# Kernel tuning notes

Measured on AMD Instinct MI355X. Metric: run time of the kernel, lower is better.

Reference implementation:

```python
import jax, jax.numpy as jnp
import numpy as np

WINDOW_LEN = 512
N_VAR = 64
LOW_RANK = 16
BATCH = 512


def setup_inputs() -> dict:
    key = jax.random.key(0)
    k_x, k_g, k_b, k_A, k_B = jax.random.split(key, 5)
    x = jax.random.normal(k_x, (BATCH, WINDOW_LEN, N_VAR, 1), dtype=jnp.float32)
    # gating initialized at gating_init in the module; use small positive values
    gating = 0.01 * jnp.ones((N_VAR,), dtype=jnp.float32)
    # bias initialized to zeros in the module, but give it random values so the
    # residual path is exercised numerically
    bias = 0.02 * jax.random.normal(k_b, (WINDOW_LEN, N_VAR), dtype=jnp.float32)
    # kaiming-uniform-ish scale for lora_A: bound = sqrt(6 / fan_in) / sqrt(1+a^2) with a=sqrt(5)
    bound = np.sqrt(6.0 / LOW_RANK) / np.sqrt(6.0)
    lora_A = jax.random.uniform(k_A, (WINDOW_LEN, LOW_RANK), dtype=jnp.float32,
                                minval=-bound, maxval=bound)
    # lora_B is zero-init in the module; use small random values for a nontrivial test
    lora_B = 0.02 * jax.random.normal(k_B, (LOW_RANK, WINDOW_LEN, N_VAR), dtype=jnp.float32)
    return {"x": x, "gating": gating, "bias": bias, "lora_A": lora_A, "lora_B": lora_B}


def reference(x, gating, bias, lora_A, lora_B):
    # x: [b, t, n, d] with t == window_len and n*d == n_var (var_wise=True path)
    b, t, n, d = x.shape
    xr = x.reshape(b, t, n * d)                     # [b, t, v]
    x1 = jnp.tanh(gating * xr)                      # gate per variable, [b, t, v]
    # Original computes weight = einsum('ik,kjl->ijl', lora_A, lora_B)  (dense [t,t,v])
    # then einsum('biv,iov->bov', x1, weight). Same math via associativity:
    tmp = jnp.einsum('biv,ik->bkv', x1, lora_A)     # [b, r, v]
    new_x = jnp.einsum('bkv,kov->bov', tmp, lora_B) # [b, t, v]
    out = xr + new_x + bias                          # residual + bias
    return out.reshape(b, t, n, d)
```

## Files before the change

kernel.cpp:

```cpp
#include <hip/hip_runtime.h>

#define WL 512
#define NV 64
#define LR 16
#define NB 512

__device__ __forceinline__ float tanh_fast(float x) {
    float e = __expf(2.0f * x);
    return 1.0f - 2.0f / (e + 1.0f);
}

__global__ __launch_bounds__(1024, 8) void k_tmp(
    const float* __restrict__ x, const float* __restrict__ gating,
    const float* __restrict__ A, float* __restrict__ tmp)
{
    __shared__ float red[16 * LR * NV];
    const int tid = threadIdx.x;
    const int b = blockIdx.x;

    const int v = tid & 63;
    const int tg = __builtin_amdgcn_readfirstlane(tid >> 6);
    const float g = gating[v];

    float acc[LR];
#pragma unroll
    for (int k = 0; k < LR; ++k) acc[k] = 0.f;

    const float* xb = x + (size_t)b * (WL * NV) + (size_t)tg * 32 * NV + v;
    const float* Abase = A + (size_t)tg * 32 * LR;

#pragma unroll 4
    for (int i = 0; i < 32; ++i) {
        const float x1 = tanh_fast(g * xb[i * NV]);
        const float* Ar = Abase + i * LR;
#pragma unroll
        for (int k = 0; k < LR; ++k) acc[k] = fmaf(x1, Ar[k], acc[k]);
    }

#pragma unroll
    for (int k = 0; k < LR; ++k) red[(tg * LR + k) * NV + v] = acc[k];
    __syncthreads();

    {
        const int p = tid;
        float s = 0.f;
#pragma unroll
        for (int t = 0; t < 16; ++t) s += red[t * (LR * NV) + p];
        tmp[(size_t)b * (LR * NV) + p] = s;
    }
}

__global__ __launch_bounds__(512, 8) void k_out(
    const float* __restrict__ x, const float* __restrict__ bias,
    const float* __restrict__ Bm, const float* __restrict__ tmp,
    float* __restrict__ out)
{
    const int tid = threadIdx.x;
    const int v = tid & 63;
    const int og = tid >> 6;
    const int o_base = blockIdx.y * 16 + og * 2;
    const int b0 = blockIdx.x * 8;

    float Breg[2][LR];
#pragma unroll
    for (int j = 0; j < 2; ++j) {
        const int o = o_base + j;
#pragma unroll
        for (int k = 0; k < LR; ++k)
            Breg[j][k] = Bm[((size_t)k * WL + o) * NV + v];
    }
    float breg[2];
#pragma unroll
    for (int j = 0; j < 2; ++j) breg[j] = bias[(o_base + j) * NV + v];

    for (int bi = 0; bi < 8; ++bi) {
        const int b = b0 + bi;
        const float* tb = tmp + (size_t)b * (LR * NV) + v;
        float tr[LR];
#pragma unroll
        for (int k = 0; k < LR; ++k) tr[k] = tb[k * NV];
        const float* xb = x + (size_t)b * WL * NV;
        float* ob = out + (size_t)b * WL * NV;
#pragma unroll
        for (int j = 0; j < 2; ++j) {
            const int o = o_base + j;
            float acc = breg[j];
#pragma unroll
            for (int k = 0; k < LR; ++k) acc += tr[k] * Breg[j][k];
            ob[o * NV + v] = xb[o * NV + v] + acc;
        }
    }
}

extern "C" void kernel_launch(void* const* d_in, const int* in_sizes, int n_in,
                              void* d_out, int out_size, void* d_ws, size_t ws_size,
                              hipStream_t stream) {
    const float* x      = (const float*)d_in[0];
    const float* gating = (const float*)d_in[1];
    const float* bias   = (const float*)d_in[2];
    const float* A      = (const float*)d_in[3];
    const float* Bm     = (const float*)d_in[4];
    float* out = (float*)d_out;
    float* tmp = (float*)d_ws;

    k_tmp<<<NB, 1024, 0, stream>>>(x, gating, A, tmp);
    k_out<<<dim3(64, 32), 512, 0, stream>>>(x, bias, Bm, tmp, out);
}
```

Measured before the change: 51.23 us.

## Retile k_out with 8 outputs per thread and double-buffered batch loads

Restructures the output kernel so each thread keeps 8 output rows of B in registers (up from 2) and handles 16 batches per block, with 4 waves per block instead of 8. Loads of tmp and x for the next batch are issued before computing the current one, a software double-buffer meant to hide global memory latency. Larger per-thread register tiles raise reuse of B and cut redundant B loads. In exchange register pressure rises and occupancy falls to 2 waves per EU, leaving fewer blocks to hide latency.

Measured after the change: 46.99 us. -8.3%, faster.

```diff
diff --git a/kernel.cpp b/kernel.cpp
--- a/kernel.cpp
+++ b/kernel.cpp
@@ -50,44 +50,84 @@
     }
 }
 
-__global__ __launch_bounds__(512, 8) void k_out(
+__global__ __attribute__((amdgpu_flat_work_group_size(256, 256),
+                          amdgpu_waves_per_eu(2, 2)))
+void k_out(
     const float* __restrict__ x, const float* __restrict__ bias,
     const float* __restrict__ Bm, const float* __restrict__ tmp,
     float* __restrict__ out)
 {
     const int tid = threadIdx.x;
     const int v = tid & 63;
-    const int og = tid >> 6;
-    const int o_base = blockIdx.y * 16 + og * 2;
-    const int b0 = blockIdx.x * 8;
+    const int w = tid >> 6;
+    const int o_base = blockIdx.y * 32 + w * 8;
+    const int b0 = blockIdx.x * 16;
 
-    float Breg[2][LR];
+    float Breg[8][LR];
 #pragma unroll
-    for (int j = 0; j < 2; ++j) {
+    for (int j = 0; j < 8; ++j) {
         const int o = o_base + j;
 #pragma unroll
         for (int k = 0; k < LR; ++k)
             Breg[j][k] = Bm[((size_t)k * WL + o) * NV + v];
     }
-    float breg[2];
+    float breg[8];
 #pragma unroll
-    for (int j = 0; j < 2; ++j) breg[j] = bias[(o_base + j) * NV + v];
+    for (int j = 0; j < 8; ++j) breg[j] = bias[(o_base + j) * NV + v];
 
-    for (int bi = 0; bi < 8; ++bi) {
+    float trA[LR], trB[LR], xrA[8], xrB[8];
+
+    {
+        const float* tb = tmp + (size_t)b0 * (LR * NV) + v;
+#pragma unroll
+        for (int k = 0; k < LR; ++k) trA[k] = tb[k * NV];
+        const float* xb = x + (size_t)b0 * WL * NV;
+#pragma unroll
+        for (int j = 0; j < 8; ++j) xrA[j] = xb[(o_base + j) * NV + v];
+    }
+
+#pragma unroll 1
+    for (int bi = 0; bi < 16; bi += 2) {
         const int b = b0 + bi;
-        const float* tb = tmp + (size_t)b * (LR * NV) + v;
-        float tr[LR];
+
+        {
+            const float* tb = tmp + (size_t)(b + 1) * (LR * NV) + v;
 #pragma unroll
-        for (int k = 0; k < LR; ++k) tr[k] = tb[k * NV];
-        const float* xb = x + (size_t)b * WL * NV;
-        float* ob = out + (size_t)b * WL * NV;
+            for (int k = 0; k < LR; ++k) trB[k] = tb[k * NV];
+            const float* xb = x + (size_t)(b + 1) * WL * NV;
 #pragma unroll
-        for (int j = 0; j < 2; ++j) {
-            const int o = o_base + j;
-            float acc = breg[j];
+            for (int j = 0; j < 8; ++j) xrB[j] = xb[(o_base + j) * NV + v];
+        }
+
+        {
+            float* ob = out + (size_t)b * WL * NV;
 #pragma unroll
-            for (int k = 0; k < LR; ++k) acc += tr[k] * Breg[j][k];
-            ob[o * NV + v] = xb[o * NV + v] + acc;
+            for (int j = 0; j < 8; ++j) {
+                float acc = breg[j];
+#pragma unroll
+                for (int k = 0; k < LR; ++k) acc += trA[k] * Breg[j][k];
+                ob[(o_base + j) * NV + v] = xrA[j] + acc;
+            }
+        }
+
+        if (bi + 2 < 16) {
+            const float* tb = tmp + (size_t)(b + 2) * (LR * NV) + v;
+#pragma unroll
+            for (int k = 0; k < LR; ++k) trA[k] = tb[k * NV];
+            const float* xb = x + (size_t)(b + 2) * WL * NV;
+#pragma unroll
+            for (int j = 0; j < 8; ++j) xrA[j] = xb[(o_base + j) * NV + v];
+        }
+
+        {
+            float* ob = out + (size_t)(b + 1) * WL * NV;
+#pragma unroll
+            for (int j = 0; j < 8; ++j) {
+                float acc = breg[j];
+#pragma unroll
+                for (int k = 0; k < LR; ++k) acc += trB[k] * Breg[j][k];
+                ob[(o_base + j) * NV + v] = xrB[j] + acc;
+            }
         }
     }
 }
@@ -104,5 +144,5 @@
     float* tmp = (float*)d_ws;
 
     k_tmp<<<NB, 1024, 0, stream>>>(x, gating, A, tmp);
-    k_out<<<dim3(64, 32), 512, 0, stream>>>(x, bias, Bm, tmp, out);
+    k_out<<<dim3(32, 16), 256, 0, stream>>>(x, bias, Bm, tmp, out);
 }
```

## Stage B and tmp tiles in LDS, prefetch x, shrink k_out blocks

Applied to the files above, without the earlier changes.

k_out now loads its B tile and the tmp rows for its batch group into shared memory using float4 global loads, then reads them per thread from LDS. The x value for the next batch is loaded one iteration early so the global load latency overlaps the current output computation. Blocks shrink to 256 threads covering 8 output rows, with twice as many blocks and a waves-per-EU hint. This adds LDS use, a block barrier and more blocks in exchange for wider, coalesced loads and fewer repeated global reads of tmp.

Measured after the change: 51.56 us. Within noise of the previous version (+0.6%).

```diff
diff --git a/kernel.cpp b/kernel.cpp
--- a/kernel.cpp
+++ b/kernel.cpp
@@ -4,6 +4,8 @@
 #define NV 64
 #define LR 16
 #define NB 512
+#define BB 8
+#define OO 8
 
 __device__ __forceinline__ float tanh_fast(float x) {
     float e = __expf(2.0f * x);
@@ -50,45 +52,79 @@
     }
 }
 
-__global__ __launch_bounds__(512, 8) void k_out(
+__global__ __attribute__((amdgpu_flat_work_group_size(256, 256),
+                          amdgpu_waves_per_eu(2, 2)))
+void k_out(
     const float* __restrict__ x, const float* __restrict__ bias,
     const float* __restrict__ Bm, const float* __restrict__ tmp,
     float* __restrict__ out)
 {
+    __shared__ float B_lds[OO * LR * NV];
+    __shared__ float T_lds[BB * LR * NV];
     const int tid = threadIdx.x;
     const int v = tid & 63;
-    const int og = tid >> 6;
-    const int o_base = blockIdx.y * 16 + og * 2;
-    const int b0 = blockIdx.x * 8;
+    const int wv = tid >> 6;
+    const int o0 = blockIdx.y * OO;
+    const int b0 = blockIdx.x * BB;
 
+#pragma unroll
+    for (int i = 0; i < 8; ++i) {
+        const int fidx = i * 256 + tid;
+        const int ko = fidx >> 4;
+        const int v4 = fidx & 15;
+        const int ol = ko >> 4;
+        const int k  = ko & 15;
+        const float4 val = *(const float4*)(Bm + ((size_t)k * WL + (o0 + ol)) * NV + v4 * 4);
+        *(float4*)(B_lds + ((ol * LR + k) * NV) + v4 * 4) = val;
+    }
+    {
+        const float4* src = (const float4*)(tmp + (size_t)b0 * (LR * NV));
+        float4* dst = (float4*)T_lds;
+#pragma unroll
+        for (int i = 0; i < 8; ++i) dst[i * 256 + tid] = src[i * 256 + tid];
+    }
+    __syncthreads();
+
+    const int ol0 = wv * 2;
     float Breg[2][LR];
 #pragma unroll
-    for (int j = 0; j < 2; ++j) {
-        const int o = o_base + j;
+    for (int j = 0; j < 2; ++j)
 #pragma unroll
         for (int k = 0; k < LR; ++k)
-            Breg[j][k] = Bm[((size_t)k * WL + o) * NV + v];
-    }
+            Breg[j][k] = B_lds[((ol0 + j) * LR + k) * NV + v];
     float breg[2];
 #pragma unroll
-    for (int j = 0; j < 2; ++j) breg[j] = bias[(o_base + j) * NV + v];
+    for (int j = 0; j < 2; ++j) breg[j] = bias[(o0 + ol0 + j) * NV + v];
 
-    for (int bi = 0; bi < 8; ++bi) {
-        const int b = b0 + bi;
-        const float* tb = tmp + (size_t)b * (LR * NV) + v;
+    float xr[2], xrn[2];
+    {
+        const float* xb = x + (size_t)b0 * (WL * NV);
+#pragma unroll
+        for (int j = 0; j < 2; ++j) xr[j] = xb[(o0 + ol0 + j) * NV + v];
+    }
+
+    for (int bl = 0; bl < BB; ++bl) {
+        const int b = b0 + bl;
+        if (bl + 1 < BB) {
+            const float* xb = x + (size_t)(b + 1) * (WL * NV);
+#pragma unroll
+            for (int j = 0; j < 2; ++j) xrn[j] = xb[(o0 + ol0 + j) * NV + v];
+        }
+
         float tr[LR];
 #pragma unroll
-        for (int k = 0; k < LR; ++k) tr[k] = tb[k * NV];
-        const float* xb = x + (size_t)b * WL * NV;
-        float* ob = out + (size_t)b * WL * NV;
+        for (int k = 0; k < LR; ++k) tr[k] = T_lds[(bl * LR + k) * NV + v];
+
+        float* ob = out + (size_t)b * (WL * NV);
 #pragma unroll
         for (int j = 0; j < 2; ++j) {
-            const int o = o_base + j;
             float acc = breg[j];
 #pragma unroll
             for (int k = 0; k < LR; ++k) acc += tr[k] * Breg[j][k];
-            ob[o * NV + v] = xb[o * NV + v] + acc;
+            ob[(o0 + ol0 + j) * NV + v] = xr[j] + acc;
         }
+
+        if (bl + 1 < BB) { xr[0] = xrn[0]; xr[1] = xrn[1]; }
     }
 }
 
@@ -104,5 +140,5 @@
     float* tmp = (float*)d_ws;
 
     k_tmp<<<NB, 1024, 0, stream>>>(x, gating, A, tmp);
-    k_out<<<dim3(64, 32), 512, 0, stream>>>(x, bias, Bm, tmp, out);
+    k_out<<<dim3(64, 64), 256, 0, stream>>>(x, bias, Bm, tmp, out);
 }
```

## Vectorize k_out with float4 lanes and double-buffer tmp loads across batches

Applied to the files above, without the earlier changes.

Rewrites the output kernel so each lane handles four variables through float4 loads and stores. Each block now covers 16 batches with 256 threads, and the tmp rows for the next batch are prefetched into registers while the current one is computed. The aim is fewer, wider memory instructions and hidden tmp load latency. The cost is higher register pressure (16 float4 for B plus two tmp buffers), with waves per EU forced to 2, which limits occupancy for a kernel bound by memory bandwidth.

After: 63.55 us. +24.0%, slower.

```diff
diff --git a/kernel.cpp b/kernel.cpp
--- a/kernel.cpp
+++ b/kernel.cpp
@@ -4,6 +4,7 @@
 #define NV 64
 #define LR 16
 #define NB 512
+#define BI 16
 
 __device__ __forceinline__ float tanh_fast(float x) {
     float e = __expf(2.0f * x);
@@ -50,44 +51,62 @@
     }
 }
 
-__global__ __launch_bounds__(512, 8) void k_out(
+__global__ __attribute__((amdgpu_flat_work_group_size(256, 256),
+                          amdgpu_waves_per_eu(2, 2)))
+void k_out(
     const float* __restrict__ x, const float* __restrict__ bias,
     const float* __restrict__ Bm, const float* __restrict__ tmp,
     float* __restrict__ out)
 {
     const int tid = threadIdx.x;
-    const int v = tid & 63;
-    const int og = tid >> 6;
-    const int o_base = blockIdx.y * 16 + og * 2;
-    const int b0 = blockIdx.x * 8;
+    const int lane = tid & 63;
+    const int w = tid >> 6;
+    const int oL = lane >> 4;
+    const int vq = lane & 15;
+    const int o = blockIdx.y * 16 + w * 4 + oL;
+    const int b0 = blockIdx.x * BI;
 
-    float Breg[2][LR];
+    float4 Breg[LR];
 #pragma unroll
-    for (int j = 0; j < 2; ++j) {
-        const int o = o_base + j;
+    for (int k = 0; k < LR; ++k)
+        Breg[k] = *(const float4*)(Bm + ((size_t)k * WL + o) * NV + vq * 4);
+
+    const float4 bias4 = *(const float4*)(bias + (size_t)o * NV + vq * 4);
+
+    float4 tA[LR], tB[LR];
+    {
+        const float* tb = tmp + (size_t)b0 * (LR * NV);
 #pragma unroll
-        for (int k = 0; k < LR; ++k)
-            Breg[j][k] = Bm[((size_t)k * WL + o) * NV + v];
+        for (int k = 0; k < LR; ++k) tA[k] = *(const float4*)(tb + k * NV + vq * 4);
     }
-    float breg[2];
+
+#pragma unroll 1
+    for (int bl = 0; bl < BI; ++bl) {
+        const int b = b0 + bl;
+
+        if (bl + 1 < BI) {
+            const float* tb = tmp + (size_t)(b + 1) * (LR * NV);
 #pragma unroll
-    for (int j = 0; j < 2; ++j) breg[j] = bias[(o_base + j) * NV + v];
+            for (int k = 0; k < LR; ++k) tB[k] = *(const float4*)(tb + k * NV + vq * 4);
+        }
 
-    for (int bi = 0; bi < 8; ++bi) {
-        const int b = b0 + bi;
-        const float* tb = tmp + (size_t)b * (LR * NV) + v;
-        float tr[LR];
+        const float4 x4 = *(const float4*)(x + (size_t)b * (WL * NV) + (size_t)o * NV + vq * 4);
+
+        float4 acc = bias4;
 #pragma unroll
-        for (int k = 0; k < LR; ++k) tr[k] = tb[k * NV];
-        const float* xb = x + (size_t)b * WL * NV;
-        float* ob = out + (size_t)b * WL * NV;
+        for (int k = 0; k < LR; ++k) {
+            acc.x = fmaf(tA[k].x, Breg[k].x, acc.x);
+            acc.y = fmaf(tA[k].y, Breg[k].y, acc.y);
+            acc.z = fmaf(tA[k].z, Breg[k].z, acc.z);
+            acc.w = fmaf(tA[k].w, Breg[k].w, acc.w);
+        }
+        acc.x += x4.x; acc.y += x4.y; acc.z += x4.z; acc.w += x4.w;
+
+        *(float4*)(out + (size_t)b * (WL * NV) + (size_t)o * NV + vq * 4) = acc;
+
+        if (bl + 1 < BI) {
 #pragma unroll
-        for (int j = 0; j < 2; ++j) {
-            const int o = o_base + j;
-            float acc = breg[j];
-#pragma unroll
-            for (int k = 0; k < LR; ++k) acc += tr[k] * Breg[j][k];
-            ob[o * NV + v] = xb[o * NV + v] + acc;
+            for (int k = 0; k < LR; ++k) tA[k] = tB[k];
         }
     }
 }
@@ -104,5 +123,5 @@
     float* tmp = (float*)d_ws;
 
     k_tmp<<<NB, 1024, 0, stream>>>(x, gating, A, tmp);
-    k_out<<<dim3(64, 32), 512, 0, stream>>>(x, bias, Bm, tmp, out);
+    k_out<<<dim3(32, 32), 256, 0, stream>>>(x, bias, Bm, tmp, out);
 }
```
